# Performance work log

Measured on AMD Instinct MI355X. Metric: run time of the kernel, lower is better.

## Reference

```python
import jax, jax.numpy as jnp
import numpy as np

D = 1024
H = 16
HD = D // H
T = 2048
B = 2
HID = 4 * D
EPS = 1e-5


def setup_inputs() -> dict:
    key = jax.random.key(0)
    ks = jax.random.split(key, 8)
    s = lambda fan_in: 1.0 / np.sqrt(fan_in)
    return {
        "x": jax.random.normal(ks[0], (B, T, D), dtype=jnp.float32),
        "ln1_g": jnp.ones((D,), jnp.float32),
        "ln1_b": jnp.zeros((D,), jnp.float32),
        "Wqkv": jax.random.uniform(ks[1], (D, 3 * D), jnp.float32, -s(D), s(D)),
        "bqkv": jnp.zeros((3 * D,), jnp.float32),
        "Wout": jax.random.uniform(ks[2], (D, D), jnp.float32, -s(D), s(D)),
        "bout": jnp.zeros((D,), jnp.float32),
        "ln2_g": jnp.ones((D,), jnp.float32),
        "ln2_b": jnp.zeros((D,), jnp.float32),
        "W1": jax.random.uniform(ks[3], (D, HID), jnp.float32, -s(D), s(D)),
        "b1": jnp.zeros((HID,), jnp.float32),
        "W2": jax.random.uniform(ks[4], (HID, D), jnp.float32, -s(HID), s(HID)),
        "b2": jnp.zeros((D,), jnp.float32),
    }


def _layernorm(h, g, b):
    mu = jnp.mean(h, axis=-1, keepdims=True)
    var = jnp.mean(jnp.square(h - mu), axis=-1, keepdims=True)
    return (h - mu) * jax.lax.rsqrt(var + EPS) * g + b


def reference(x, ln1_g, ln1_b, Wqkv, bqkv, Wout, bout, ln2_g, ln2_b, W1, b1, W2, b2):
    b, t, d = x.shape
    scale = 1.0 / np.sqrt(HD)

    # --- attention (pre-LN) ---
    h = _layernorm(x, ln1_g, ln1_b)
    qkv = h @ Wqkv + bqkv                      # [b, t, 3d]
    q, k, v = jnp.split(qkv, 3, axis=-1)
    q = q.reshape(b, t, H, HD)
    k = k.reshape(b, t, H, HD)
    v = v.reshape(b, t, H, HD)
    scores = jnp.einsum("bqhd,bkhd->bhqk", q, k) * scale  # [b, h, t, t]
    causal = jnp.tril(jnp.ones((t, t), dtype=bool))
    scores = jnp.where(causal, scores, -jnp.inf)
    attn = jax.nn.softmax(scores, axis=-1)
    out = jnp.einsum("bhqk,bkhd->bqhd", attn, v).reshape(b, t, d)
    x = x + (out @ Wout + bout)

    # --- MLP (pre-LN) ---
    h = _layernorm(x, ln2_g, ln2_b)
    h = jax.nn.gelu(h @ W1 + b1, approximate=False)
    x = x + (h @ W2 + b2)
    return x
```

## Files before the change

kernel.cpp:

```cpp
#include <hip/hip_runtime.h>
#include <hip/hip_bf16.h>
#include <math.h>

#define DD 1024
#define TT 2048
#define BB 2
#define HH 16
#define HDIM 64
#define HIDD 4096

typedef __attribute__((ext_vector_type(4))) float f32x4;
typedef __attribute__((ext_vector_type(8))) __bf16 bf16x8;
typedef __attribute__((ext_vector_type(4))) __bf16 bf16x4;

#define MF16 __builtin_amdgcn_mfma_f32_16x16x32_bf16

__device__ __forceinline__ void gload_lds16(const void* g, void* l) {
  __builtin_amdgcn_global_load_lds(
      (const __attribute__((address_space(1))) void*)g,
      (__attribute__((address_space(3))) void*)l, 16, 0, 0);
}

__global__ __launch_bounds__(256) void castAll(const float* __restrict__ Wqkv,
                                               const float* __restrict__ Wout,
                                               const float* __restrict__ W1,
                                               const float* __restrict__ W2,
                                               __bf16* __restrict__ WqkvT,
                                               __bf16* __restrict__ WoutT,
                                               __bf16* __restrict__ W1T,
                                               __bf16* __restrict__ W2T) {
  const int id = blockIdx.x;
  const float* W;
  __bf16* Wt;
  int K, N, gx, local;
  if (id < 768)        { W = Wqkv; Wt = WqkvT; K = 1024; N = 3072; gx = 48; local = id; }
  else if (id < 1024)  { W = Wout; Wt = WoutT; K = 1024; N = 1024; gx = 16; local = id - 768; }
  else if (id < 2048)  { W = W1;   Wt = W1T;   K = 1024; N = 4096; gx = 64; local = id - 1024; }
  else                 { W = W2;   Wt = W2T;   K = 4096; N = 1024; gx = 16; local = id - 2048; }
  const int n0 = (local % gx) * 64, k0 = (local / gx) * 64;
  __shared__ float t[64][65];
#pragma unroll
  for (int e = 0; e < 16; ++e) {
    int idx = e * 256 + threadIdx.x;
    int rr = idx >> 6, cc = idx & 63;
    t[rr][cc] = W[(size_t)(k0 + rr) * N + n0 + cc];
  }
  __syncthreads();
#pragma unroll
  for (int e = 0; e < 16; ++e) {
    int idx = e * 256 + threadIdx.x;
    int rr = idx >> 6, cc = idx & 63;
    Wt[(size_t)(n0 + rr) * K + k0 + cc] = (__bf16)t[cc][rr];
  }
}

__global__ __launch_bounds__(256) void ln_fwd(const float* __restrict__ x,
                                              const float* __restrict__ gamma,
                                              const float* __restrict__ beta,
                                              __bf16* __restrict__ out) {
  const int wave = threadIdx.x >> 6, lane = threadIdx.x & 63;
  const int row = blockIdx.x * 4 + wave;
  const float* xr = x + (size_t)row * DD;
  float4 v[4];
  float s = 0.0f, ss = 0.0f;
#pragma unroll
  for (int c = 0; c < 4; ++c) {
    v[c] = reinterpret_cast<const float4*>(xr)[c * 64 + lane];
    s += v[c].x + v[c].y + v[c].z + v[c].w;
    ss += v[c].x * v[c].x + v[c].y * v[c].y + v[c].z * v[c].z + v[c].w * v[c].w;
  }
#pragma unroll
  for (int m = 1; m <= 32; m <<= 1) { s += __shfl_xor(s, m); ss += __shfl_xor(ss, m); }
  const float mu = s * (1.0f / DD);
  const float rs = rsqrtf(ss * (1.0f / DD) - mu * mu + 1e-5f);
#pragma unroll
  for (int c = 0; c < 4; ++c) {
    const float4 gm = reinterpret_cast<const float4*>(gamma)[c * 64 + lane];
    const float4 bt = reinterpret_cast<const float4*>(beta)[c * 64 + lane];
    bf16x4 o;
    o[0] = (__bf16)((v[c].x - mu) * rs * gm.x + bt.x);
    o[1] = (__bf16)((v[c].y - mu) * rs * gm.y + bt.y);
    o[2] = (__bf16)((v[c].z - mu) * rs * gm.z + bt.z);
    o[3] = (__bf16)((v[c].w - mu) * rs * gm.w + bt.w);
    *reinterpret_cast<bf16x4*>(out + (size_t)row * DD + (c * 64 + lane) * 4) = o;
  }
}

template <int MODE>
__global__ __launch_bounds__(512, 1) void gemm8(const __bf16* __restrict__ A,
                                                const __bf16* __restrict__ Bt,
                                                const float* __restrict__ bias,
                                                void* __restrict__ out0,
                                                __bf16* __restrict__ q1,
                                                __bf16* __restrict__ q2,
                                                __bf16* __restrict__ q3,
                                                int N, int K, int kchunk) {
  const int tid = threadIdx.x;
  const int wid = tid >> 6, lane = tid & 63;
  const int g = lane >> 4, r = lane & 15;
  const int wrh = wid >> 2;
  const int wc = (wid & 3) * 64;

  int bm, bn, kbase, zz;
  if constexpr (MODE == 3) {
    const int L = blockIdx.x;
    const int xcd = L & 7, idx = L >> 3;
    zz = xcd >> 1;
    bm = (((xcd & 1) << 3) + (idx >> 2)) * 256;
    bn = (idx & 3) * 256;
    kbase = zz * kchunk;
  } else {
    const int gx = gridDim.x;
    const int nwg = gx * gridDim.y;
    const int orig = blockIdx.y * gx + blockIdx.x;
    const int swz = (orig & 7) * (nwg >> 3) + (orig >> 3);
    const int bn4 = swz & 3;
    const int bmt = (swz >> 2) % gx;
    const int bng = (swz >> 2) / gx;
    bm = bmt * 256;
    bn = (bng * 4 + bn4) * 256;
    kbase = 0;
    zz = 0;
  }

  const int NT = kchunk >> 6;
  const __bf16* Asrc = A + (size_t)bm * K + kbase;
  const __bf16* Bsrc = Bt + (size_t)bn * K + kbase;

  __shared__ __bf16 lds[2][4][8192];

  f32x4 acc[8][4] = {};
  bf16x8 bfr[4][2];

  auto STG = [&](int ab, int h, int kt) {
    const __bf16* src = (ab ? Bsrc : Asrc) + (size_t)h * 128 * K;
    char* dst = (char*)&lds[kt & 1][ab * 2 + h][0];
#pragma unroll
    for (int gl = 0; gl < 2; ++gl) {
      const int o = gl * 8192 + wid * 1024 + lane * 16;
      const int row = o >> 7;
      const int cbs = (o & 127) ^ (((row >> 2) & 1) << 5);
      gload_lds16((const char*)src + (size_t)row * (K * 2) + kt * 128 + cbs,
                  dst + gl * 8192 + wid * 1024);
    }
  };
  auto DSA = [&](int s, int mi, int kk) -> bf16x8 {
    return *(const bf16x8*)((const char*)&lds[s][wrh][0] + (mi * 16 + r) * 128 +
                            ((kk * 64 + g * 16) ^ ((r & 4) << 3)));
  };
  auto DSB = [&](int s, int nj, int kk) -> bf16x8 {
    const int rt = wc + nj * 16 + r;
    return *(const bf16x8*)((const char*)&lds[s][2 + (rt >> 7)][0] + (rt & 127) * 128 +
                            ((kk * 64 + g * 16) ^ ((r & 4) << 3)));
  };

#define PH(S, Q, STAGE_STMT, WAIT_STMT)                                        \
  {                                                                            \
    if (Q == 0) {                                                              \
      _Pragma("unroll") for (int nj = 0; nj < 4; ++nj) {                       \
        bfr[nj][0] = DSB(S, nj, 0);                                            \
        bfr[nj][1] = DSB(S, nj, 1);                                            \
      }                                                                        \
    }                                                                          \
    bf16x8 a00 = DSA(S, 2 * Q, 0), a01 = DSA(S, 2 * Q, 1);                     \
    bf16x8 a10 = DSA(S, 2 * Q + 1, 0), a11 = DSA(S, 2 * Q + 1, 1);             \
    STAGE_STMT;                                                                \
    WAIT_STMT;                                                                 \
    __builtin_amdgcn_s_barrier();                                              \
    asm volatile("s_waitcnt lgkmcnt(0)" ::: "memory");                         \
    __builtin_amdgcn_s_setprio(1);                                             \
    _Pragma("unroll") for (int nj = 0; nj < 4; ++nj) {                         \
      acc[2 * Q][nj] = MF16(a00, bfr[nj][0], acc[2 * Q][nj], 0, 0, 0);         \
      acc[2 * Q][nj] = MF16(a01, bfr[nj][1], acc[2 * Q][nj], 0, 0, 0);         \
      acc[2 * Q + 1][nj] = MF16(a10, bfr[nj][0], acc[2 * Q + 1][nj], 0, 0, 0); \
      acc[2 * Q + 1][nj] = MF16(a11, bfr[nj][1], acc[2 * Q + 1][nj], 0, 0, 0); \
    }                                                                          \
    __builtin_amdgcn_s_setprio(0);                                             \
    __builtin_amdgcn_s_barrier();                                              \
  }

  STG(1, 0, 0); STG(1, 1, 0); STG(0, 0, 0); STG(0, 1, 0);
  STG(1, 0, 1); STG(1, 1, 1); STG(0, 0, 1);
  asm volatile("s_waitcnt vmcnt(6)" ::: "memory");
  __builtin_amdgcn_s_barrier();

  const int NI = NT >> 1;
  for (int i = 0; i < NI; ++i) {
    const int k2 = 2 * i + 2, k3 = 2 * i + 3;
    const bool nl = (i + 1 < NI);
    PH(0, 0, { STG(0, 1, 2 * i + 1); }, {});
    PH(0, 1, { if (nl) STG(1, 0, k2); }, {});
    PH(0, 2, { if (nl) STG(1, 1, k2); }, {});
    PH(0, 3, { if (nl) STG(0, 0, k2); },
       { if (nl) asm volatile("s_waitcnt vmcnt(6)" ::: "memory");
         else    asm volatile("s_waitcnt vmcnt(0)" ::: "memory"); });
    PH(1, 0, { if (nl) STG(0, 1, k2); }, {});
    PH(1, 1, { if (nl) STG(1, 0, k3); }, {});
    PH(1, 2, { if (nl) STG(1, 1, k3); }, {});
    PH(1, 3, { if (nl) STG(0, 0, k3); },
       { if (nl) asm volatile("s_waitcnt vmcnt(6)" ::: "memory"); });
  }
#undef PH

  const int row0 = bm + wrh * 128 + g * 4;
  const int col0 = bn + wc + r;
#pragma unroll
  for (int mi = 0; mi < 8; ++mi) {
#pragma unroll
    for (int nj = 0; nj < 4; ++nj) {
      const int col = col0 + nj * 16;
      float bv = 0.0f;
      if constexpr (MODE != 3) bv = bias[col];
#pragma unroll
      for (int i4 = 0; i4 < 4; ++i4) {
        const int rowg = row0 + mi * 16 + i4;
        const size_t idx = (size_t)rowg * N + col;
        const float v = acc[mi][nj][i4];
        if constexpr (MODE == 0) {
          ((__bf16*)out0)[idx] = (__bf16)(v + bv);
        } else if constexpr (MODE == 2) {
          const float t = v + bv;
          const float u2 = t * (1.5957691216f + t * t * 0.0713548163f);
          ((__bf16*)out0)[idx] = (__bf16)(t * __builtin_amdgcn_rcpf(1.0f + __expf(-u2)));
        } else {
          if (zz == 0) {
            ((float*)out0)[idx] = v;
          } else {
            __bf16* p = (zz == 1 ? q1 : (zz == 2 ? q2 : q3));
            p[idx] = (__bf16)v;
          }
        }
      }
    }
  }
}

__global__ __launch_bounds__(256) void reduceW2(const __bf16* __restrict__ p1,
                                                const __bf16* __restrict__ p2,
                                                const __bf16* __restrict__ p3,
                                                const float* __restrict__ x1,
                                                const float* __restrict__ b2,
                                                float* __restrict__ out) {
  const size_t i8 = ((size_t)blockIdx.x * 256 + threadIdx.x) * 8;
  const int col0 = (int)(i8 & 1023);
  bf16x8 a = *(const bf16x8*)(p1 + i8);
  bf16x8 b = *(const bf16x8*)(p2 + i8);
  bf16x8 c = *(const bf16x8*)(p3 + i8);
  float4 o0 = *(const float4*)(out + i8);
  float4 o1 = *(const float4*)(out + i8 + 4);
  const float4 xv0 = *(const float4*)(x1 + i8);
  const float4 xv1 = *(const float4*)(x1 + i8 + 4);
  const float4 bb0 = *(const float4*)(b2 + col0);
  const float4 bb1 = *(const float4*)(b2 + col0 + 4);
  float* op0 = (float*)&o0;
  float* op1 = (float*)&o1;
  const float* xp0 = (const float*)&xv0;
  const float* xp1 = (const float*)&xv1;
  const float* bp0 = (const float*)&bb0;
  const float* bp1 = (const float*)&bb1;
#pragma unroll
  for (int j = 0; j < 4; ++j)
    op0[j] += xp0[j] + bp0[j] + (float)a[j] + (float)b[j] + (float)c[j];
#pragma unroll
  for (int j = 0; j < 4; ++j)
    op1[j] += xp1[j] + bp1[j] + (float)a[4 + j] + (float)b[4 + j] + (float)c[4 + j];
  *(float4*)(out + i8) = o0;
  *(float4*)(out + i8 + 4) = o1;
}

template <int MODE>
__global__ __launch_bounds__(256) void gemm_bt(const __bf16* __restrict__ A,
                                               const __bf16* __restrict__ Bt,
                                               const float* __restrict__ bias,
                                               const float* __restrict__ resid,
                                               void* __restrict__ Cout,
                                               int M, int N, int K) {
  __shared__ __bf16 As[128 * 32];
  __shared__ __bf16 Bs[128 * 32];
  const int tid = threadIdx.x;
  const int wave = tid >> 6, lane = tid & 63;
  const int g = lane >> 4, r = lane & 15;
  const int gx = gridDim.x;
  const int nwg = gx * gridDim.y;
  const int orig = blockIdx.y * gx + blockIdx.x;
  const int swz = (orig & 7) * (nwg >> 3) + (orig >> 3);
  const int bn4 = swz & 3;
  const int bmt = (swz >> 2) % gx;
  const int bng = (swz >> 2) / gx;
  const int bm = bmt * 128;
  const int bn = (bng * 4 + bn4) * 128;
  const int wr = (wave >> 1) * 64, wc = (wave & 1) * 64;
  f32x4 acc[4][4] = {};

  const int off0 = wave * 2048 + lane * 16;
  const int off1 = off0 + 1024;
  const int sr0 = off0 >> 6, sk0 = (off0 & 63) >> 1;
  const int sr1 = off1 >> 6, sk1 = (off1 & 63) >> 1;
  const __bf16* gA0 = A + (size_t)(bm + sr0) * K + sk0;
  const __bf16* gA1 = A + (size_t)(bm + sr1) * K + sk1;
  const __bf16* gB0 = Bt + (size_t)(bn + sr0) * K + sk0;
  const __bf16* gB1 = Bt + (size_t)(bn + sr1) * K + sk1;
  char* lA0 = (char*)As + wave * 2048;
  char* lA1 = lA0 + 1024;
  char* lB0 = (char*)Bs + wave * 2048;
  char* lB1 = lB0 + 1024;

  for (int k0 = 0; k0 < K; k0 += 32) {
    gload_lds16(gA0 + k0, lA0);
    gload_lds16(gA1 + k0, lA1);
    gload_lds16(gB0 + k0, lB0);
    gload_lds16(gB1 + k0, lB1);
    __syncthreads();
    bf16x8 af[4], bf[4];
#pragma unroll
    for (int mi = 0; mi < 4; ++mi)
      af[mi] = *reinterpret_cast<const bf16x8*>(&As[(wr + mi * 16 + r) * 32 + g * 8]);
#pragma unroll
    for (int ni = 0; ni < 4; ++ni)
      bf[ni] = *reinterpret_cast<const bf16x8*>(&Bs[(wc + ni * 16 + r) * 32 + g * 8]);
    __builtin_amdgcn_s_setprio(1);
#pragma unroll
    for (int mi = 0; mi < 4; ++mi)
#pragma unroll
      for (int ni = 0; ni < 4; ++ni)
        acc[mi][ni] = MF16(af[mi], bf[ni], acc[mi][ni], 0, 0, 0);
    __builtin_amdgcn_s_setprio(0);
    __syncthreads();
  }

  const int row0 = bm + wr + 4 * g;
  const int col0 = bn + wc + r;
#pragma unroll
  for (int mi = 0; mi < 4; ++mi) {
#pragma unroll
    for (int ni = 0; ni < 4; ++ni) {
      const int col = col0 + ni * 16;
      const float bv = bias[col];
#pragma unroll
      for (int i = 0; i < 4; ++i) {
        const int row = row0 + mi * 16 + i;
        const size_t idx = (size_t)row * N + col;
        float v = acc[mi][ni][i] + bv;
        if (MODE == 0) {
          ((__bf16*)Cout)[idx] = (__bf16)v;
        } else if (MODE == 1) {
          ((float*)Cout)[idx] = v + resid[idx];
        } else {
          const float u2 = v * (1.5957691216f + v * v * 0.0713548163f);
          const float gl = v * __builtin_amdgcn_rcpf(1.0f + __expf(-u2));
          ((__bf16*)Cout)[idx] = (__bf16)gl;
        }
      }
    }
  }
}

__global__ __launch_bounds__(256) void vtrans(const __bf16* __restrict__ qkv,
                                              __bf16* __restrict__ vtg) {
  const int bh = blockIdx.y, b = bh >> 4, h = bh & 15;
  const int t0 = blockIdx.x * 64;
  const int tid = threadIdx.x, wave = tid >> 6, lane = tid & 63;
  __shared__ __bf16 tile[64 * 64];
#pragma unroll
  for (int e = 0; e < 2; ++e) {
    const int gid = e * 256 + tid;
    const int row = gid >> 3, d0 = (gid & 7) * 8;
    bf16x8 v = *reinterpret_cast<const bf16x8*>(
        qkv + (size_t)(b * TT + t0 + row) * 3072 + 2048 + h * 64 + d0);
    const int slot = (d0 >> 3) ^ (row & 7);
    *reinterpret_cast<bf16x8*>((char*)tile + row * 128 + slot * 16) = v;
  }
  __syncthreads();
  const int d = lane;
#pragma unroll
  for (int e = 0; e < 2; ++e) {
    const int k0 = (wave * 2 + e) * 8;
    bf16x8 o;
#pragma unroll
    for (int j = 0; j < 8; ++j) {
      const int row = k0 + j;
      o[j] = *(const __bf16*)((const char*)tile + row * 128 +
                              (((d >> 3) ^ (row & 7)) << 4) + (d & 7) * 2);
    }
    *reinterpret_cast<bf16x8*>(&vtg[((size_t)bh * 64 + d) * 2048 + t0 + k0]) = o;
  }
}

__device__ __forceinline__ void stage_kv(const __bf16* __restrict__ src_row0, int rstride,
                                         int wave, int lane, char* tile) {
#pragma unroll
  for (int qq = 0; qq < 2; ++qq) {
    const int o = wave * 2048 + qq * 1024 + lane * 16;
    const int p = o >> 12, row = (o >> 6) & 63, cb = (o >> 4) & 3;
    gload_lds16(src_row0 + (size_t)row * rstride + p * 32 + cb * 8,
                tile + wave * 2048 + qq * 1024);
  }
}

__global__ __launch_bounds__(256) void attn_fwd(const __bf16* __restrict__ qkv,
                                                const __bf16* __restrict__ vtg,
                                                __bf16* __restrict__ atto) {
  const int orig = blockIdx.y * gridDim.x + blockIdx.x;
  const int swz = (orig & 7) * 64 + (orig >> 3);
  const int bh = swz >> 4;
  const int j = swz & 15;
  const int b = bh >> 4, h = bh & 15;
  const int tid = threadIdx.x;
  const int wave = tid >> 6, lane = tid & 63;
  const int g = lane >> 4, r = lane & 15;

  __shared__ __bf16 Qs[2 * 64 * 32];
  __shared__ __bf16 Ks[2][2 * 64 * 32];
  __shared__ __bf16 Vs[2][2 * 64 * 32];
  __shared__ __bf16 Pl[4][2 * 16 * 32];

  const __bf16* ksrc = qkv + (size_t)(b * TT) * 3072 + 1024 + h * 64;
  const __bf16* vsrc = vtg + (size_t)bh * 64 * 2048;
  const float C2 = 0.18033688011112042f;

  for (int ph = 0; ph < 2; ++ph) {
    const int qt = ph ? (31 - j) : j;
    const int q0 = qt * 64;
    stage_kv(qkv + (size_t)(b * TT + q0) * 3072 + h * 64, 3072, wave, lane, (char*)Qs);
    stage_kv(ksrc, 3072, wave, lane, (char*)Ks[0]);
    stage_kv(vsrc, 2048, wave, lane, (char*)Vs[0]);

    f32x4 oacc[4] = {};
    float m_s[4], l_s[4];
#pragma unroll
    for (int i = 0; i < 4; ++i) { m_s[i] = -1e30f; l_s[i] = 0.0f; }

    const int nt = qt + 1;
    int cur = 0;
    for (int t = 0; t < nt; ++t) {
      const int kv0 = t * 64;
      __syncthreads();
      if (t + 1 < nt) {
        stage_kv(ksrc + (size_t)(kv0 + 64) * 3072, 3072, wave, lane, (char*)Ks[cur ^ 1]);
        stage_kv(vsrc + kv0 + 64, 2048, wave, lane, (char*)Vs[cur ^ 1]);
      }
      bf16x8 qf[2];
#pragma unroll
      for (int kp = 0; kp < 2; ++kp)
        qf[kp] = *reinterpret_cast<const bf16x8*>(&Qs[kp * 2048 + (wave * 16 + r) * 32 + g * 8]);
      f32x4 s[4];
#pragma unroll
      for (int cn = 0; cn < 4; ++cn) s[cn] = f32x4{0.f, 0.f, 0.f, 0.f};
      __builtin_amdgcn_s_setprio(1);
#pragma unroll
      for (int cn = 0; cn < 4; ++cn)
#pragma unroll
        for (int kp = 0; kp < 2; ++kp) {
          bf16x8 bk = *reinterpret_cast<const bf16x8*>(
              &Ks[cur][kp * 2048 + (cn * 16 + r) * 32 + g * 8]);
          s[cn] = MF16(qf[kp], bk, s[cn], 0, 0, 0);
        }
      __builtin_amdgcn_s_setprio(0);
      const int rowg = q0 + wave * 16 + 4 * g;
      float pm[4];
#pragma unroll
      for (int i = 0; i < 4; ++i) pm[i] = -1e30f;
      if (kv0 + 63 > q0 + wave * 16) {
#pragma unroll
        for (int cn = 0; cn < 4; ++cn) {
          const int colg = kv0 + cn * 16 + r;
#pragma unroll
          for (int i = 0; i < 4; ++i) {
            float v = s[cn][i] * C2;
            v = (colg > rowg + i) ? -1e30f : v;
            s[cn][i] = v;
            pm[i] = fmaxf(pm[i], v);
          }
        }
      } else {
#pragma unroll
        for (int cn = 0; cn < 4; ++cn)
#pragma unroll
          for (int i = 0; i < 4; ++i) {
            const float v = s[cn][i] * C2;
            s[cn][i] = v;
            pm[i] = fmaxf(pm[i], v);
          }
      }
      const int upd = __any((pm[0] > m_s[0] + 8.0f) || (pm[1] > m_s[1] + 8.0f) ||
                            (pm[2] > m_s[2] + 8.0f) || (pm[3] > m_s[3] + 8.0f));
      if (upd) {
#pragma unroll
        for (int i = 0; i < 4; ++i) {
          pm[i] = fmaxf(pm[i], __shfl_xor(pm[i], 1));
          pm[i] = fmaxf(pm[i], __shfl_xor(pm[i], 2));
          pm[i] = fmaxf(pm[i], __shfl_xor(pm[i], 4));
          pm[i] = fmaxf(pm[i], __shfl_xor(pm[i], 8));
          const float mn = fmaxf(m_s[i], pm[i]);
          const float sf = __builtin_amdgcn_exp2f(m_s[i] - mn);
          m_s[i] = mn;
          l_s[i] *= sf;
#pragma unroll
          for (int ni = 0; ni < 4; ++ni) oacc[ni][i] *= sf;
        }
      }
#pragma unroll
      for (int cn = 0; cn < 4; ++cn)
#pragma unroll
        for (int i = 0; i < 4; ++i) {
          const float p = __builtin_amdgcn_exp2f(s[cn][i] - m_s[i]);
          s[cn][i] = p;
          l_s[i] += p;
        }
#pragma unroll
      for (int cn = 0; cn < 4; ++cn)
#pragma unroll
        for (int i = 0; i < 4; ++i) {
          const int row = 4 * g + i;
          const int byteoff = (cn >> 1) * 1024 +
              ((row * 64 + (cn & 1) * 32 + r * 2) ^ ((row & 7) << 4));
          *(__bf16*)((char*)&Pl[wave][0] + byteoff) = (__bf16)s[cn][i];
        }
      bf16x8 pa[2];
#pragma unroll
      for (int kp = 0; kp < 2; ++kp) {
        const int byteoff = kp * 1024 + ((r * 64 + g * 16) ^ ((r & 7) << 4));
        pa[kp] = *reinterpret_cast<const bf16x8*>((const char*)&Pl[wave][0] + byteoff);
      }
      __builtin_amdgcn_s_setprio(1);
#pragma unroll
      for (int ni = 0; ni < 4; ++ni)
#pragma unroll
        for (int kp = 0; kp < 2; ++kp) {
          bf16x8 bv = *reinterpret_cast<const bf16x8*>(
              &Vs[cur][kp * 2048 + (ni * 16 + r) * 32 + g * 8]);
          oacc[ni] = MF16(pa[kp], bv, oacc[ni], 0, 0, 0);
        }
      __builtin_amdgcn_s_setprio(0);
      cur ^= 1;
    }

#pragma unroll
    for (int i = 0; i < 4; ++i) {
      float l = l_s[i];
      l += __shfl_xor(l, 1);
      l += __shfl_xor(l, 2);
      l += __shfl_xor(l, 4);
      l += __shfl_xor(l, 8);
      const float inv = 1.0f / l;
      const size_t rowo = (size_t)(b * TT + q0 + wave * 16 + 4 * g + i) * DD + h * 64;
#pragma unroll
      for (int ni = 0; ni < 4; ++ni)
        atto[rowo + ni * 16 + r] = (__bf16)(oacc[ni][i] * inv);
    }
    __syncthreads();
  }
}

extern "C" void kernel_launch(void* const* d_in, const int* in_sizes, int n_in,
                              void* d_out, int out_size, void* d_ws, size_t ws_size,
                              hipStream_t stream) {
  const float* x     = (const float*)d_in[0];
  const float* ln1_g = (const float*)d_in[1];
  const float* ln1_b = (const float*)d_in[2];
  const float* Wqkv  = (const float*)d_in[3];
  const float* bqkv  = (const float*)d_in[4];
  const float* Wout  = (const float*)d_in[5];
  const float* bout  = (const float*)d_in[6];
  const float* ln2_g = (const float*)d_in[7];
  const float* ln2_b = (const float*)d_in[8];
  const float* W1    = (const float*)d_in[9];
  const float* b1    = (const float*)d_in[10];
  const float* W2    = (const float*)d_in[11];
  const float* b2    = (const float*)d_in[12];
  float* out = (float*)d_out;

  char* ws = (char*)d_ws;
  const size_t MB = 1024 * 1024;
  __bf16* WqkvT = (__bf16*)(ws);
  __bf16* WoutT = (__bf16*)(ws + 6 * MB);
  __bf16* W1T   = (__bf16*)(ws + 8 * MB);
  __bf16* W2T   = (__bf16*)(ws + 16 * MB);
  float*  x1    = (float*)(ws + 24 * MB);
  __bf16* vtg   = (__bf16*)(ws + 24 * MB);
  __bf16* hbuf  = (__bf16*)(ws + 40 * MB);
  __bf16* qkvb  = (__bf16*)(ws + 48 * MB);
  __bf16* atto  = (__bf16*)(ws + 72 * MB);
  __bf16* mlp1  = (__bf16*)(ws + 48 * MB);
  __bf16* p1b   = (__bf16*)(ws);
  __bf16* p2b   = (__bf16*)(ws + 8 * MB);
  __bf16* p3b   = (__bf16*)(ws + 40 * MB);

  castAll<<<3072, 256, 0, stream>>>(Wqkv, Wout, W1, W2, WqkvT, WoutT, W1T, W2T);

  ln_fwd<<<1024, 256, 0, stream>>>(x, ln1_g, ln1_b, hbuf);
  gemm8<0><<<dim3(16, 12), 512, 0, stream>>>(hbuf, WqkvT, bqkv, qkvb,
                                             nullptr, nullptr, nullptr, 3072, 1024, 1024);
  vtrans<<<dim3(32, 32), 256, 0, stream>>>(qkvb, vtg);
  attn_fwd<<<dim3(16, 32), 256, 0, stream>>>(qkvb, vtg, atto);
  gemm_bt<1><<<dim3(32, 8), 256, 0, stream>>>(atto, WoutT, bout, x, x1, 4096, 1024, 1024);

  ln_fwd<<<1024, 256, 0, stream>>>(x1, ln2_g, ln2_b, hbuf);
  gemm8<2><<<dim3(16, 16), 512, 0, stream>>>(hbuf, W1T, b1, mlp1,
                                             nullptr, nullptr, nullptr, 4096, 1024, 1024);
  gemm8<3><<<dim3(256, 1), 512, 0, stream>>>(mlp1, W2T, nullptr, out,
                                             p1b, p2b, p3b, 1024, 4096, 1024);
  reduceW2<<<2048, 256, 0, stream>>>(p1b, p2b, p3b, x1, b2, out);
}
```

Baseline: 233.3 us.

## Move split-K W2 GEMM from 256-tile gemm8 to 128-tile gemm_bt kernel

The split-K MLP down-projection now uses the simpler 128x128-tile gemm_bt kernel (1024 blocks) instead of the pipelined 256x256-tile gemm8 (256 blocks). The XCD-aware mapping and the four K-chunk partial outputs are kept, with the split-K logic moved into gemm_bt. This raises block count and occupancy across CUs, but gives up gemm8's deeper LDS double-buffered pipeline and larger data reuse per tile.

```diff
diff --git a/kernel.cpp b/kernel.cpp
--- a/kernel.cpp
+++ b/kernel.cpp
@@ -91,9 +91,6 @@
                                                 const __bf16* __restrict__ Bt,
                                                 const float* __restrict__ bias,
                                                 void* __restrict__ out0,
-                                                __bf16* __restrict__ q1,
-                                                __bf16* __restrict__ q2,
-                                                __bf16* __restrict__ q3,
                                                 int N, int K, int kchunk) {
   const int tid = threadIdx.x;
   const int wid = tid >> 6, lane = tid & 63;
@@ -101,31 +98,19 @@
   const int wrh = wid >> 2;
   const int wc = (wid & 3) * 64;
 
-  int bm, bn, kbase, zz;
-  if constexpr (MODE == 3) {
-    const int L = blockIdx.x;
-    const int xcd = L & 7, idx = L >> 3;
-    zz = xcd >> 1;
-    bm = (((xcd & 1) << 3) + (idx >> 2)) * 256;
-    bn = (idx & 3) * 256;
-    kbase = zz * kchunk;
-  } else {
-    const int gx = gridDim.x;
-    const int nwg = gx * gridDim.y;
-    const int orig = blockIdx.y * gx + blockIdx.x;
-    const int swz = (orig & 7) * (nwg >> 3) + (orig >> 3);
-    const int bn4 = swz & 3;
-    const int bmt = (swz >> 2) % gx;
-    const int bng = (swz >> 2) / gx;
-    bm = bmt * 256;
-    bn = (bng * 4 + bn4) * 256;
-    kbase = 0;
-    zz = 0;
-  }
+  const int gx = gridDim.x;
+  const int nwg = gx * gridDim.y;
+  const int orig = blockIdx.y * gx + blockIdx.x;
+  const int swz = (orig & 7) * (nwg >> 3) + (orig >> 3);
+  const int bn4 = swz & 3;
+  const int bmt = (swz >> 2) % gx;
+  const int bng = (swz >> 2) / gx;
+  const int bm = bmt * 256;
+  const int bn = (bng * 4 + bn4) * 256;
 
   const int NT = kchunk >> 6;
-  const __bf16* Asrc = A + (size_t)bm * K + kbase;
-  const __bf16* Bsrc = Bt + (size_t)bn * K + kbase;
+  const __bf16* Asrc = A + (size_t)bm * K;
+  const __bf16* Bsrc = Bt + (size_t)bn * K;
 
   __shared__ __bf16 lds[2][4][8192];
 
@@ -209,8 +194,7 @@
 #pragma unroll
     for (int nj = 0; nj < 4; ++nj) {
       const int col = col0 + nj * 16;
-      float bv = 0.0f;
-      if constexpr (MODE != 3) bv = bias[col];
+      const float bv = bias[col];
 #pragma unroll
       for (int i4 = 0; i4 < 4; ++i4) {
         const int rowg = row0 + mi * 16 + i4;
@@ -218,17 +202,10 @@
         const float v = acc[mi][nj][i4];
         if constexpr (MODE == 0) {
           ((__bf16*)out0)[idx] = (__bf16)(v + bv);
-        } else if constexpr (MODE == 2) {
+        } else {
           const float t = v + bv;
           const float u2 = t * (1.5957691216f + t * t * 0.0713548163f);
           ((__bf16*)out0)[idx] = (__bf16)(t * __builtin_amdgcn_rcpf(1.0f + __expf(-u2)));
-        } else {
-          if (zz == 0) {
-            ((float*)out0)[idx] = v;
-          } else {
-            __bf16* p = (zz == 1 ? q1 : (zz == 2 ? q2 : q3));
-            p[idx] = (__bf16)v;
-          }
         }
       }
     }
@@ -274,21 +251,39 @@
                                                const float* __restrict__ bias,
                                                const float* __restrict__ resid,
                                                void* __restrict__ Cout,
+                                               __bf16* __restrict__ q1,
+                                               __bf16* __restrict__ q2,
+                                               __bf16* __restrict__ q3,
                                                int M, int N, int K) {
   __shared__ __bf16 As[128 * 32];
   __shared__ __bf16 Bs[128 * 32];
   const int tid = threadIdx.x;
   const int wave = tid >> 6, lane = tid & 63;
   const int g = lane >> 4, r = lane & 15;
-  const int gx = gridDim.x;
-  const int nwg = gx * gridDim.y;
-  const int orig = blockIdx.y * gx + blockIdx.x;
-  const int swz = (orig & 7) * (nwg >> 3) + (orig >> 3);
-  const int bn4 = swz & 3;
-  const int bmt = (swz >> 2) % gx;
-  const int bng = (swz >> 2) / gx;
-  const int bm = bmt * 128;
-  const int bn = (bng * 4 + bn4) * 128;
+  int bm, bn, kbase, kcnt, zz;
+  if constexpr (MODE == 3) {
+    const int L = blockIdx.x;
+    const int xcd = L & 7, idx = L >> 3;
+    zz = xcd >> 1;
+    const int bmh = xcd & 1;
+    bm = ((bmh << 4) + (idx >> 3)) * 128;
+    bn = (idx & 7) * 128;
+    kbase = zz * 1024;
+    kcnt = 1024;
+  } else {
+    const int gx = gridDim.x;
+    const int nwg = gx * gridDim.y;
+    const int orig = blockIdx.y * gx + blockIdx.x;
+    const int swz = (orig & 7) * (nwg >> 3) + (orig >> 3);
+    const int bn4 = swz & 3;
+    const int bmt = (swz >> 2) % gx;
+    const int bng = (swz >> 2) / gx;
+    bm = bmt * 128;
+    bn = (bng * 4 + bn4) * 128;
+    kbase = 0;
+    kcnt = K;
+    zz = 0;
+  }
   const int wr = (wave >> 1) * 64, wc = (wave & 1) * 64;
   f32x4 acc[4][4] = {};
 
@@ -296,16 +291,16 @@
   const int off1 = off0 + 1024;
   const int sr0 = off0 >> 6, sk0 = (off0 & 63) >> 1;
   const int sr1 = off1 >> 6, sk1 = (off1 & 63) >> 1;
-  const __bf16* gA0 = A + (size_t)(bm + sr0) * K + sk0;
-  const __bf16* gA1 = A + (size_t)(bm + sr1) * K + sk1;
-  const __bf16* gB0 = Bt + (size_t)(bn + sr0) * K + sk0;
-  const __bf16* gB1 = Bt + (size_t)(bn + sr1) * K + sk1;
+  const __bf16* gA0 = A + (size_t)(bm + sr0) * K + kbase + sk0;
+  const __bf16* gA1 = A + (size_t)(bm + sr1) * K + kbase + sk1;
+  const __bf16* gB0 = Bt + (size_t)(bn + sr0) * K + kbase + sk0;
+  const __bf16* gB1 = Bt + (size_t)(bn + sr1) * K + kbase + sk1;
   char* lA0 = (char*)As + wave * 2048;
   char* lA1 = lA0 + 1024;
   char* lB0 = (char*)Bs + wave * 2048;
   char* lB1 = lB0 + 1024;
 
-  for (int k0 = 0; k0 < K; k0 += 32) {
+  for (int k0 = 0; k0 < kcnt; k0 += 32) {
     gload_lds16(gA0 + k0, lA0);
     gload_lds16(gA1 + k0, lA1);
     gload_lds16(gB0 + k0, lB0);
@@ -335,16 +330,24 @@
 #pragma unroll
     for (int ni = 0; ni < 4; ++ni) {
       const int col = col0 + ni * 16;
-      const float bv = bias[col];
+      float bv = 0.0f;
+      if constexpr (MODE != 3) bv = bias[col];
 #pragma unroll
       for (int i = 0; i < 4; ++i) {
         const int row = row0 + mi * 16 + i;
         const size_t idx = (size_t)row * N + col;
         float v = acc[mi][ni][i] + bv;
-        if (MODE == 0) {
+        if constexpr (MODE == 0) {
           ((__bf16*)Cout)[idx] = (__bf16)v;
-        } else if (MODE == 1) {
+        } else if constexpr (MODE == 1) {
           ((float*)Cout)[idx] = v + resid[idx];
+        } else if constexpr (MODE == 3) {
+          if (zz == 0) {
+            ((float*)Cout)[idx] = v;
+          } else {
+            __bf16* p = (zz == 1 ? q1 : (zz == 2 ? q2 : q3));
+            p[idx] = (__bf16)v;
+          }
         } else {
           const float u2 = v * (1.5957691216f + v * v * 0.0713548163f);
           const float gl = v * __builtin_amdgcn_rcpf(1.0f + __expf(-u2));
@@ -589,16 +592,15 @@
   castAll<<<3072, 256, 0, stream>>>(Wqkv, Wout, W1, W2, WqkvT, WoutT, W1T, W2T);
 
   ln_fwd<<<1024, 256, 0, stream>>>(x, ln1_g, ln1_b, hbuf);
-  gemm8<0><<<dim3(16, 12), 512, 0, stream>>>(hbuf, WqkvT, bqkv, qkvb,
-                                             nullptr, nullptr, nullptr, 3072, 1024, 1024);
+  gemm8<0><<<dim3(16, 12), 512, 0, stream>>>(hbuf, WqkvT, bqkv, qkvb, 3072, 1024, 1024);
   vtrans<<<dim3(32, 32), 256, 0, stream>>>(qkvb, vtg);
   attn_fwd<<<dim3(16, 32), 256, 0, stream>>>(qkvb, vtg, atto);
-  gemm_bt<1><<<dim3(32, 8), 256, 0, stream>>>(atto, WoutT, bout, x, x1, 4096, 1024, 1024);
+  gemm_bt<1><<<dim3(32, 8), 256, 0, stream>>>(atto, WoutT, bout, x, x1,
+                                              nullptr, nullptr, nullptr, 4096, 1024, 1024);
 
   ln_fwd<<<1024, 256, 0, stream>>>(x1, ln2_g, ln2_b, hbuf);
-  gemm8<2><<<dim3(16, 16), 512, 0, stream>>>(hbuf, W1T, b1, mlp1,
-                                             nullptr, nullptr, nullptr, 4096, 1024, 1024);
-  gemm8<3><<<dim3(256, 1), 512, 0, stream>>>(mlp1, W2T, nullptr, out,
-                                             p1b, p2b, p3b, 1024, 4096, 1024);
+  gemm8<2><<<dim3(16, 16), 512, 0, stream>>>(hbuf, W1T, b1, mlp1, 4096, 1024, 1024);
+  gemm_bt<3><<<1024, 256, 0, stream>>>(mlp1, W2T, nullptr, nullptr, out,
+                                       p1b, p2b, p3b, 4096, 1024, 4096);
   reduceW2<<<2048, 256, 0, stream>>>(p1b, p2b, p3b, x1, b2, out);
 }
```

Result: slower. 247.1 us (+5.9%).
